# Kernel tuning notes

Hardware: AMD Instinct MI355X
Metric: run time of the kernel (lower is better)

The kernel has to match this reference:

```python
import jax, jax.numpy as jnp
import numpy as np

B, IN_DIM, OUT_DIM, N_KNOTS = 8192, 1024, 1024, 4


def setup_inputs() -> dict:
    key = jax.random.key(0)
    k_feat, k_phase, k_w = jax.random.split(key, 3)
    feats = jax.random.normal(k_feat, (B, IN_DIM), dtype=jnp.float32)
    phase = jax.random.uniform(k_phase, (B, 1), dtype=jnp.float32)  # phase in [0,1)
    x = jnp.concatenate([feats, phase], axis=1)  # [B, IN_DIM+1]
    bound = np.sqrt(6.0 / (OUT_DIM * IN_DIM))
    weight_knots = jax.random.uniform(
        k_w, (N_KNOTS, OUT_DIM, IN_DIM), dtype=jnp.float32, minval=-bound, maxval=bound)
    bias_knots = jnp.zeros((N_KNOTS, OUT_DIM), dtype=jnp.float32)
    return {"x": x, "weight_knots": weight_knots, "bias_knots": bias_knots}


def _cubic(y, mu):
    # Catmull-Rom cubic blend over the 4 gathered knots, y: [B,4,D], mu: [B,1]
    y0, y1, y2, y3 = y[:, 0], y[:, 1], y[:, 2], y[:, 3]
    return ((-0.5 * y0 + 1.5 * y1 - 1.5 * y2 + 0.5 * y3) * mu * mu * mu
            + (y0 - 2.5 * y1 + 2.0 * y2 - 0.5 * y3) * mu * mu
            + (-0.5 * y0 + 0.5 * y2) * mu + y1)


def reference(x, weight_knots, bias_knots):
    K = weight_knots.shape[0]
    phase = x[:, -1]            # [B]
    feats = x[:, :-1]           # [B, IN_DIM]
    pscale = K * phase
    mu = jnp.mod(pscale, 1.0)[:, None]                       # [B, 1]
    i1 = jnp.mod(pscale.astype(jnp.int32), K)
    idx = jnp.stack([jnp.mod(i1 - 1, K), i1,
                     jnp.mod(i1 + 1, K), jnp.mod(i1 + 2, K)], axis=1)  # [B, 4]
    # Exploit linearity: matvec against each knot matrix once, then blend.
    # Mathematically identical to cubic(W0,..,W3) @ feats + cubic(b0,..,b3).
    yk = jnp.einsum('koi,bi->bko', weight_knots, feats)      # [B, K, OUT]
    y4 = jnp.take_along_axis(yk, idx[:, :, None], axis=1)    # [B, 4, OUT]
    b4 = bias_knots[idx]                                     # [B, 4, OUT]
    res = _cubic(y4 + b4, mu)                                # cubic is linear in y
    return jax.nn.elu(res)
```

## Files before the change

kernel.cpp:

```cpp
#include <hip/hip_runtime.h>
#include <math.h>

#define IN_DIM 1024
#define OUT_DIM 1024
#define NROWS 8192
#define KDIM 4096

typedef __attribute__((ext_vector_type(8))) short bf16x8;
typedef __attribute__((ext_vector_type(4))) float f32x4;

static __device__ __forceinline__ unsigned short f2bf(float f) {
  union { float f; unsigned u; } v; v.f = f;
  unsigned u = v.u;
  return (unsigned short)((u + 0x7fffu + ((u >> 16) & 1u)) >> 16);
}

__global__ __launch_bounds__(256) void prep_a_kernel(
    const float* __restrict__ x, unsigned short* __restrict__ A4,
    float* __restrict__ coef)
{
  const int b = blockIdx.x;
  const float* xr = x + (size_t)b * (IN_DIM + 1);
  const float phase = xr[IN_DIM];
  const float ps = 4.0f * phase;
  const int ip = (int)ps;
  const int i1 = ip & 3;
  const float mu = ps - (float)ip;
  const float mu2 = mu * mu, mu3 = mu2 * mu;
  const float c0 = -0.5f * mu3 +        mu2 - 0.5f * mu;
  const float c1 =  1.5f * mu3 - 2.5f * mu2 + 1.0f;
  const float c2 = -1.5f * mu3 + 2.0f * mu2 + 0.5f * mu;
  const float c3 =  0.5f * mu3 - 0.5f * mu2;
  const int d0 = (0 - i1) & 3, d1 = (1 - i1) & 3, d2 = (2 - i1) & 3, d3 = (3 - i1) & 3;
  const float w0 = d0 == 0 ? c1 : d0 == 1 ? c2 : d0 == 2 ? c3 : c0;
  const float w1 = d1 == 0 ? c1 : d1 == 1 ? c2 : d1 == 2 ? c3 : c0;
  const float w2 = d2 == 0 ? c1 : d2 == 1 ? c2 : d2 == 2 ? c3 : c0;
  const float w3 = d3 == 0 ? c1 : d3 == 1 ? c2 : d3 == 2 ? c3 : c0;
  if (threadIdx.x == 0) {
    float4 cv; cv.x = w0; cv.y = w1; cv.z = w2; cv.w = w3;
    *reinterpret_cast<float4*>(coef + (size_t)b * 4) = cv;
  }

  const int i = threadIdx.x * 4;
  const float f0 = xr[i], f1 = xr[i + 1], f2 = xr[i + 2], f3 = xr[i + 3];
  unsigned short* arow = A4 + (size_t)b * KDIM;
  ushort4 vv;
  vv.x = f2bf(w0 * f0); vv.y = f2bf(w0 * f1); vv.z = f2bf(w0 * f2); vv.w = f2bf(w0 * f3);
  *reinterpret_cast<ushort4*>(arow + 0 * IN_DIM + i) = vv;
  vv.x = f2bf(w1 * f0); vv.y = f2bf(w1 * f1); vv.z = f2bf(w1 * f2); vv.w = f2bf(w1 * f3);
  *reinterpret_cast<ushort4*>(arow + 1 * IN_DIM + i) = vv;
  vv.x = f2bf(w2 * f0); vv.y = f2bf(w2 * f1); vv.z = f2bf(w2 * f2); vv.w = f2bf(w2 * f3);
  *reinterpret_cast<ushort4*>(arow + 2 * IN_DIM + i) = vv;
  vv.x = f2bf(w3 * f0); vv.y = f2bf(w3 * f1); vv.z = f2bf(w3 * f2); vv.w = f2bf(w3 * f3);
  *reinterpret_cast<ushort4*>(arow + 3 * IN_DIM + i) = vv;
}

__global__ __launch_bounds__(256) void prep_w_kernel(
    const float* __restrict__ W, unsigned short* __restrict__ Wb)
{
  const int t = blockIdx.x * 256 + threadIdx.x;
  const int flat = t * 4;
  const int k = flat >> 20;
  const int o = (flat >> 10) & 1023;
  const int i = flat & 1023;
  const float4 f = *reinterpret_cast<const float4*>(W + flat);
  ushort4 vv;
  vv.x = f2bf(f.x); vv.y = f2bf(f.y); vv.z = f2bf(f.z); vv.w = f2bf(f.w);
  *reinterpret_cast<ushort4*>(Wb + (size_t)o * KDIM + k * IN_DIM + i) = vv;
}

#define BM 128
#define BN 128
#define BK 64

__global__ __launch_bounds__(256, 2) void gemm_kernel(
    const unsigned short* __restrict__ A4,
    const unsigned short* __restrict__ Wb,
    const float* __restrict__ coef,
    const float* __restrict__ bias,
    float* __restrict__ out)
{
  __shared__ unsigned short As[BM * BK];
  __shared__ unsigned short Bs[BN * BK];

  const int tid  = threadIdx.x;
  const int wave = tid >> 6;
  const int lane = tid & 63;
  const int row0 = blockIdx.y * BM;
  const int col0 = blockIdx.x * BN;

  const int srow = tid >> 3;
  const int scc  = tid & 7;
  const int sgc  = (scc ^ (srow & 7)) * 8;

  const int wr  = (wave >> 1) * 64;
  const int wc  = (wave & 1) * 64;
  const int fm  = lane & 15;
  const int fq  = lane >> 4;

  f32x4 acc[4][4];
  const f32x4 zero = {0.f, 0.f, 0.f, 0.f};
  #pragma unroll
  for (int a = 0; a < 4; a++)
    #pragma unroll
    for (int b = 0; b < 4; b++)
      acc[a][b] = zero;

  const unsigned short* Abase = A4 + (size_t)row0 * KDIM;
  const unsigned short* Bbase = Wb + (size_t)col0 * KDIM;

  for (int kb = 0; kb < KDIM; kb += BK) {
    #pragma unroll
    for (int it = 0; it < 4; it++) {
      const int r = srow + it * 32;
      __builtin_amdgcn_global_load_lds(
          (const __attribute__((address_space(1))) void*)(Abase + (size_t)r * KDIM + kb + sgc),
          (__attribute__((address_space(3))) void*)(As + r * BK + scc * 8), 16, 0, 0);
      __builtin_amdgcn_global_load_lds(
          (const __attribute__((address_space(1))) void*)(Bbase + (size_t)r * KDIM + kb + sgc),
          (__attribute__((address_space(3))) void*)(Bs + r * BK + scc * 8), 16, 0, 0);
    }
    __syncthreads();

    #pragma unroll
    for (int kk = 0; kk < BK; kk += 32) {
      bf16x8 af[4], bfr[4];
      #pragma unroll
      for (int mi = 0; mi < 4; mi++) {
        const int r = wr + mi * 16 + fm;
        const int lc = ((kk >> 3) + fq) ^ (fm & 7);
        af[mi] = *reinterpret_cast<const bf16x8*>(As + r * BK + lc * 8);
      }
      #pragma unroll
      for (int ni = 0; ni < 4; ni++) {
        const int r = wc + ni * 16 + fm;
        const int lc = ((kk >> 3) + fq) ^ (fm & 7);
        bfr[ni] = *reinterpret_cast<const bf16x8*>(Bs + r * BK + lc * 8);
      }
      #pragma unroll
      for (int mi = 0; mi < 4; mi++)
        #pragma unroll
        for (int ni = 0; ni < 4; ni++)
          acc[mi][ni] = __builtin_amdgcn_mfma_f32_16x16x32_bf16(
              af[mi], bfr[ni], acc[mi][ni], 0, 0, 0);
    }
    __syncthreads();
  }

  #pragma unroll
  for (int mi = 0; mi < 4; mi++) {
    const int rbase = row0 + wr + mi * 16 + (fq << 2);
    const float4 cf0 = *reinterpret_cast<const float4*>(coef + (size_t)(rbase + 0) * 4);
    const float4 cf1 = *reinterpret_cast<const float4*>(coef + (size_t)(rbase + 1) * 4);
    const float4 cf2 = *reinterpret_cast<const float4*>(coef + (size_t)(rbase + 2) * 4);
    const float4 cf3 = *reinterpret_cast<const float4*>(coef + (size_t)(rbase + 3) * 4);
    const float4 cfs[4] = {cf0, cf1, cf2, cf3};
    #pragma unroll
    for (int ni = 0; ni < 4; ni++) {
      const int col = col0 + wc + ni * 16 + fm;
      const float b0 = bias[col];
      const float b1 = bias[OUT_DIM + col];
      const float b2 = bias[2 * OUT_DIM + col];
      const float b3 = bias[3 * OUT_DIM + col];
      #pragma unroll
      for (int r = 0; r < 4; r++) {
        float v = acc[mi][ni][r]
                + cfs[r].x * b0 + cfs[r].y * b1 + cfs[r].z * b2 + cfs[r].w * b3;
        v = (v > 0.0f) ? v : expm1f(v);
        out[(size_t)(rbase + r) * OUT_DIM + col] = v;
      }
    }
  }
}

extern "C" void kernel_launch(void* const* d_in, const int* in_sizes, int n_in,
                              void* d_out, int out_size, void* d_ws, size_t ws_size,
                              hipStream_t stream) {
  const float* x  = (const float*)d_in[0];
  const float* wk = (const float*)d_in[1];
  const float* bk = (const float*)d_in[2];
  float* out = (float*)d_out;

  char* ws = (char*)d_ws;
  float* coef          = (float*)ws;
  unsigned short* Wb   = (unsigned short*)(ws + (128u << 10));
  unsigned short* A4   = (unsigned short*)(ws + (128u << 10) + (8u << 20));

  hipLaunchKernelGGL(prep_a_kernel, dim3(NROWS), dim3(256), 0, stream, x, A4, coef);
  hipLaunchKernelGGL(prep_w_kernel, dim3(4096), dim3(256), 0, stream, wk, Wb);
  hipLaunchKernelGGL(gemm_kernel, dim3(OUT_DIM / BN, NROWS / BM), dim3(256), 0, stream,
                     A4, Wb, coef, bk, out);
}
```

Measured before the change: 190.8 us.

## Build scaled A tiles in GEMM from a bf16 feature copy instead of materializing A4

New measurement: 182.2 us. 1.05x faster.

```diff
diff --git a/kernel.cpp b/kernel.cpp
--- a/kernel.cpp
+++ b/kernel.cpp
@@ -4,7 +4,7 @@
 #define IN_DIM 1024
 #define OUT_DIM 1024
 #define NROWS 8192
-#define KDIM 4096
+#define XSTRIDE 1025
 
 typedef __attribute__((ext_vector_type(8))) short bf16x8;
 typedef __attribute__((ext_vector_type(4))) float f32x4;
@@ -15,58 +15,30 @@
   return (unsigned short)((u + 0x7fffu + ((u >> 16) & 1u)) >> 16);
 }
 
-__global__ __launch_bounds__(256) void prep_a_kernel(
-    const float* __restrict__ x, unsigned short* __restrict__ A4,
-    float* __restrict__ coef)
+__global__ __launch_bounds__(256) void prep_kernel(
+    const float* __restrict__ x, const float* __restrict__ W,
+    unsigned short* __restrict__ Wb, unsigned short* __restrict__ F)
 {
-  const int b = blockIdx.x;
-  const float* xr = x + (size_t)b * (IN_DIM + 1);
-  const float phase = xr[IN_DIM];
-  const float ps = 4.0f * phase;
-  const int ip = (int)ps;
-  const int i1 = ip & 3;
-  const float mu = ps - (float)ip;
-  const float mu2 = mu * mu, mu3 = mu2 * mu;
-  const float c0 = -0.5f * mu3 +        mu2 - 0.5f * mu;
-  const float c1 =  1.5f * mu3 - 2.5f * mu2 + 1.0f;
-  const float c2 = -1.5f * mu3 + 2.0f * mu2 + 0.5f * mu;
-  const float c3 =  0.5f * mu3 - 0.5f * mu2;
-  const int d0 = (0 - i1) & 3, d1 = (1 - i1) & 3, d2 = (2 - i1) & 3, d3 = (3 - i1) & 3;
-  const float w0 = d0 == 0 ? c1 : d0 == 1 ? c2 : d0 == 2 ? c3 : c0;
-  const float w1 = d1 == 0 ? c1 : d1 == 1 ? c2 : d1 == 2 ? c3 : c0;
-  const float w2 = d2 == 0 ? c1 : d2 == 1 ? c2 : d2 == 2 ? c3 : c0;
-  const float w3 = d3 == 0 ? c1 : d3 == 1 ? c2 : d3 == 2 ? c3 : c0;
-  if (threadIdx.x == 0) {
-    float4 cv; cv.x = w0; cv.y = w1; cv.z = w2; cv.w = w3;
-    *reinterpret_cast<float4*>(coef + (size_t)b * 4) = cv;
-  }
-
-  const int i = threadIdx.x * 4;
-  const float f0 = xr[i], f1 = xr[i + 1], f2 = xr[i + 2], f3 = xr[i + 3];
-  unsigned short* arow = A4 + (size_t)b * KDIM;
-  ushort4 vv;
-  vv.x = f2bf(w0 * f0); vv.y = f2bf(w0 * f1); vv.z = f2bf(w0 * f2); vv.w = f2bf(w0 * f3);
-  *reinterpret_cast<ushort4*>(arow + 0 * IN_DIM + i) = vv;
-  vv.x = f2bf(w1 * f0); vv.y = f2bf(w1 * f1); vv.z = f2bf(w1 * f2); vv.w = f2bf(w1 * f3);
-  *reinterpret_cast<ushort4*>(arow + 1 * IN_DIM + i) = vv;
-  vv.x = f2bf(w2 * f0); vv.y = f2bf(w2 * f1); vv.z = f2bf(w2 * f2); vv.w = f2bf(w2 * f3);
-  *reinterpret_cast<ushort4*>(arow + 2 * IN_DIM + i) = vv;
-  vv.x = f2bf(w3 * f0); vv.y = f2bf(w3 * f1); vv.z = f2bf(w3 * f2); vv.w = f2bf(w3 * f3);
-  *reinterpret_cast<ushort4*>(arow + 3 * IN_DIM + i) = vv;
-}
-
-__global__ __launch_bounds__(256) void prep_w_kernel(
-    const float* __restrict__ W, unsigned short* __restrict__ Wb)
-{
-  const int t = blockIdx.x * 256 + threadIdx.x;
-  const int flat = t * 4;
-  const int k = flat >> 20;
-  const int o = (flat >> 10) & 1023;
-  const int i = flat & 1023;
-  const float4 f = *reinterpret_cast<const float4*>(W + flat);
-  ushort4 vv;
-  vv.x = f2bf(f.x); vv.y = f2bf(f.y); vv.z = f2bf(f.z); vv.w = f2bf(f.w);
-  *reinterpret_cast<ushort4*>(Wb + (size_t)o * KDIM + k * IN_DIM + i) = vv;
+  const int blk = blockIdx.x;
+  if (blk < 4096) {
+    const int t = blk * 256 + threadIdx.x;
+    const int flat = t * 4;
+    const int k = flat >> 20;
+    const int o = (flat >> 10) & 1023;
+    const int i = flat & 1023;
+    const float4 f = *reinterpret_cast<const float4*>(W + flat);
+    ushort4 vv;
+    vv.x = f2bf(f.x); vv.y = f2bf(f.y); vv.z = f2bf(f.z); vv.w = f2bf(f.w);
+    *reinterpret_cast<ushort4*>(Wb + (size_t)o * 4096 + k * 1024 + i) = vv;
+  } else {
+    const int b = blk - 4096;
+    const float* xr = x + (size_t)b * XSTRIDE;
+    const int i = threadIdx.x * 4;
+    ushort4 vv;
+    vv.x = f2bf(xr[i]); vv.y = f2bf(xr[i + 1]);
+    vv.z = f2bf(xr[i + 2]); vv.w = f2bf(xr[i + 3]);
+    *reinterpret_cast<ushort4*>(F + (size_t)b * 1024 + i) = vv;
+  }
 }
 
 #define BM 128
@@ -74,14 +46,15 @@
 #define BK 64
 
 __global__ __launch_bounds__(256, 2) void gemm_kernel(
-    const unsigned short* __restrict__ A4,
+    const unsigned short* __restrict__ F,
     const unsigned short* __restrict__ Wb,
-    const float* __restrict__ coef,
+    const float* __restrict__ x,
     const float* __restrict__ bias,
     float* __restrict__ out)
 {
   __shared__ unsigned short As[BM * BK];
   __shared__ unsigned short Bs[BN * BK];
+  __shared__ float cfs[BM][4];
 
   const int tid  = threadIdx.x;
   const int wave = tid >> 6;
@@ -89,14 +62,39 @@
   const int row0 = blockIdx.y * BM;
   const int col0 = blockIdx.x * BN;
 
+  if (tid < BM) {
+    const float phase = x[(size_t)(row0 + tid) * XSTRIDE + IN_DIM];
+    const float ps = 4.0f * phase;
+    const int ip = (int)ps;
+    const int i1 = ip & 3;
+    const float mu = ps - (float)ip;
+    const float mu2 = mu * mu, mu3 = mu2 * mu;
+    const float c0 = -0.5f * mu3 +        mu2 - 0.5f * mu;
+    const float c1 =  1.5f * mu3 - 2.5f * mu2 + 1.0f;
+    const float c2 = -1.5f * mu3 + 2.0f * mu2 + 0.5f * mu;
+    const float c3 =  0.5f * mu3 - 0.5f * mu2;
+    const int d0 = (0 - i1) & 3, d1 = (1 - i1) & 3, d2 = (2 - i1) & 3, d3 = (3 - i1) & 3;
+    float4 cv;
+    cv.x = d0 == 0 ? c1 : d0 == 1 ? c2 : d0 == 2 ? c3 : c0;
+    cv.y = d1 == 0 ? c1 : d1 == 1 ? c2 : d1 == 2 ? c3 : c0;
+    cv.z = d2 == 0 ? c1 : d2 == 1 ? c2 : d2 == 2 ? c3 : c0;
+    cv.w = d3 == 0 ? c1 : d3 == 1 ? c2 : d3 == 2 ? c3 : c0;
+    *reinterpret_cast<float4*>(cfs[tid]) = cv;
+  }
+  __syncthreads();
+
+  const int ar  = tid >> 1;
+  const int ac0 = (tid & 1) * 32;
+  const float4 cfr = *reinterpret_cast<const float4*>(cfs[ar]);
+
   const int srow = tid >> 3;
   const int scc  = tid & 7;
   const int sgc  = (scc ^ (srow & 7)) * 8;
 
-  const int wr  = (wave >> 1) * 64;
-  const int wc  = (wave & 1) * 64;
-  const int fm  = lane & 15;
-  const int fq  = lane >> 4;
+  const int wr = (wave >> 1) * 64;
+  const int wc = (wave & 1) * 64;
+  const int fm = lane & 15;
+  const int fq = lane >> 4;
 
   f32x4 acc[4][4];
   const f32x4 zero = {0.f, 0.f, 0.f, 0.f};
@@ -106,55 +104,79 @@
     for (int b = 0; b < 4; b++)
       acc[a][b] = zero;
 
-  const unsigned short* Abase = A4 + (size_t)row0 * KDIM;
-  const unsigned short* Bbase = Wb + (size_t)col0 * KDIM;
-
-  for (int kb = 0; kb < KDIM; kb += BK) {
-    #pragma unroll
-    for (int it = 0; it < 4; it++) {
-      const int r = srow + it * 32;
-      __builtin_amdgcn_global_load_lds(
-          (const __attribute__((address_space(1))) void*)(Abase + (size_t)r * KDIM + kb + sgc),
-          (__attribute__((address_space(3))) void*)(As + r * BK + scc * 8), 16, 0, 0);
-      __builtin_amdgcn_global_load_lds(
-          (const __attribute__((address_space(1))) void*)(Bbase + (size_t)r * KDIM + kb + sgc),
-          (__attribute__((address_space(3))) void*)(Bs + r * BK + scc * 8), 16, 0, 0);
+  const unsigned short* Arow  = F + (size_t)(row0 + ar) * 1024 + ac0;
+  const unsigned short* Bbase = Wb + (size_t)col0 * 4096;
+
+  for (int kb0 = 0; kb0 < 1024; kb0 += BK) {
+    uint4 araw[4];
+    #pragma unroll
+    for (int m = 0; m < 4; m++)
+      araw[m] = *reinterpret_cast<const uint4*>(Arow + kb0 + m * 8);
+
+    #pragma unroll
+    for (int k = 0; k < 4; k++) {
+      const float ck = (k == 0) ? cfr.x : (k == 1) ? cfr.y : (k == 2) ? cfr.z : cfr.w;
+      #pragma unroll
+      for (int m = 0; m < 4; m++) {
+        uint4 d = araw[m];
+        uint4 r;
+        #pragma unroll
+        for (int j = 0; j < 4; j++) {
+          const unsigned dj = (&d.x)[j];
+          float lo = __uint_as_float(dj << 16);
+          float hi = __uint_as_float(dj & 0xffff0000u);
+          lo *= ck; hi *= ck;
+          const unsigned lr = __float_as_uint(lo) + 0x8000u;
+          const unsigned hr = __float_as_uint(hi) + 0x8000u;
+          (&r.x)[j] = __builtin_amdgcn_perm(hr, lr, 0x07060302u);
+        }
+        const int gc = (ac0 >> 3) + m;
+        const int slot = gc ^ (ar & 7);
+        *reinterpret_cast<uint4*>(As + ar * BK + slot * 8) = r;
+      }
+      #pragma unroll
+      for (int it = 0; it < 4; it++) {
+        const int rr = srow + it * 32;
+        __builtin_amdgcn_global_load_lds(
+            (const __attribute__((address_space(1))) void*)(Bbase + (size_t)rr * 4096 + k * 1024 + kb0 + sgc),
+            (__attribute__((address_space(3))) void*)(Bs + rr * BK + scc * 8), 16, 0, 0);
+      }
+      __syncthreads();
+
+      #pragma unroll
+      for (int kk = 0; kk < BK; kk += 32) {
+        bf16x8 af[4], bfr[4];
+        #pragma unroll
+        for (int mi = 0; mi < 4; mi++) {
+          const int r = wr + mi * 16 + fm;
+          const int lc = ((kk >> 3) + fq) ^ (fm & 7);
+          af[mi] = *reinterpret_cast<const bf16x8*>(As + r * BK + lc * 8);
+        }
+        #pragma unroll
+        for (int ni = 0; ni < 4; ni++) {
+          const int r = wc + ni * 16 + fm;
+          const int lc = ((kk >> 3) + fq) ^ (fm & 7);
+          bfr[ni] = *reinterpret_cast<const bf16x8*>(Bs + r * BK + lc * 8);
+        }
+        #pragma unroll
+        for (int mi = 0; mi < 4; mi++)
+          #pragma unroll
+          for (int ni = 0; ni < 4; ni++)
+            acc[mi][ni] = __builtin_amdgcn_mfma_f32_16x16x32_bf16(
+                af[mi], bfr[ni], acc[mi][ni], 0, 0, 0);
+      }
+      __syncthreads();
     }
-    __syncthreads();
-
-    #pragma unroll
-    for (int kk = 0; kk < BK; kk += 32) {
-      bf16x8 af[4], bfr[4];
-      #pragma unroll
-      for (int mi = 0; mi < 4; mi++) {
-        const int r = wr + mi * 16 + fm;
-        const int lc = ((kk >> 3) + fq) ^ (fm & 7);
-        af[mi] = *reinterpret_cast<const bf16x8*>(As + r * BK + lc * 8);
-      }
-      #pragma unroll
-      for (int ni = 0; ni < 4; ni++) {
-        const int r = wc + ni * 16 + fm;
-        const int lc = ((kk >> 3) + fq) ^ (fm & 7);
-        bfr[ni] = *reinterpret_cast<const bf16x8*>(Bs + r * BK + lc * 8);
-      }
-      #pragma unroll
-      for (int mi = 0; mi < 4; mi++)
-        #pragma unroll
-        for (int ni = 0; ni < 4; ni++)
-          acc[mi][ni] = __builtin_amdgcn_mfma_f32_16x16x32_bf16(
-              af[mi], bfr[ni], acc[mi][ni], 0, 0, 0);
-    }
-    __syncthreads();
   }
 
   #pragma unroll
   for (int mi = 0; mi < 4; mi++) {
-    const int rbase = row0 + wr + mi * 16 + (fq << 2);
-    const float4 cf0 = *reinterpret_cast<const float4*>(coef + (size_t)(rbase + 0) * 4);
-    const float4 cf1 = *reinterpret_cast<const float4*>(coef + (size_t)(rbase + 1) * 4);
-    const float4 cf2 = *reinterpret_cast<const float4*>(coef + (size_t)(rbase + 2) * 4);
-    const float4 cf3 = *reinterpret_cast<const float4*>(coef + (size_t)(rbase + 3) * 4);
-    const float4 cfs[4] = {cf0, cf1, cf2, cf3};
+    const int rloc = wr + mi * 16 + (fq << 2);
+    const int rbase = row0 + rloc;
+    float4 cfs4[4];
+    #pragma unroll
+    for (int r = 0; r < 4; r++)
+      cfs4[r] = *reinterpret_cast<const float4*>(cfs[rloc + r]);
     #pragma unroll
     for (int ni = 0; ni < 4; ni++) {
       const int col = col0 + wc + ni * 16 + fm;
@@ -165,7 +187,7 @@
       #pragma unroll
       for (int r = 0; r < 4; r++) {
         float v = acc[mi][ni][r]
-                + cfs[r].x * b0 + cfs[r].y * b1 + cfs[r].z * b2 + cfs[r].w * b3;
+                + cfs4[r].x * b0 + cfs4[r].y * b1 + cfs4[r].z * b2 + cfs4[r].w * b3;
         v = (v > 0.0f) ? v : expm1f(v);
         out[(size_t)(rbase + r) * OUT_DIM + col] = v;
       }
@@ -182,12 +204,10 @@
   float* out = (float*)d_out;
 
   char* ws = (char*)d_ws;
-  float* coef          = (float*)ws;
-  unsigned short* Wb   = (unsigned short*)(ws + (128u << 10));
-  unsigned short* A4   = (unsigned short*)(ws + (128u << 10) + (8u << 20));
-
-  hipLaunchKernelGGL(prep_a_kernel, dim3(NROWS), dim3(256), 0, stream, x, A4, coef);
-  hipLaunchKernelGGL(prep_w_kernel, dim3(4096), dim3(256), 0, stream, wk, Wb);
+  unsigned short* Wb = (unsigned short*)ws;
+  unsigned short* F  = (unsigned short*)(ws + (16u << 20));
+
+  hipLaunchKernelGGL(prep_kernel, dim3(4096 + NROWS), dim3(256), 0, stream, x, wk, Wb, F);
   hipLaunchKernelGGL(gemm_kernel, dim3(OUT_DIM / BN, NROWS / BM), dim3(256), 0, stream,
-                     A4, Wb, coef, bk, out);
-}
+                     F, Wb, x, bk, out);
+}
```

## Blend knot outputs in epilogue instead of scaling inputs along K

Applied to the files above, without the earlier changes.

Result: faster. 161.3 us (-15.4%).

```diff
diff --git a/kernel.cpp b/kernel.cpp
--- a/kernel.cpp
+++ b/kernel.cpp
@@ -4,77 +4,73 @@
 #define IN_DIM 1024
 #define OUT_DIM 1024
 #define NROWS 8192
-#define KDIM 4096
+#define XSTRIDE 1025
 
 typedef __attribute__((ext_vector_type(8))) short bf16x8;
 typedef __attribute__((ext_vector_type(4))) float f32x4;
 
-static __device__ __forceinline__ unsigned short f2bf(float f) {
+static __device__ __forceinline__ unsigned f2bf(float f) {
   union { float f; unsigned u; } v; v.f = f;
   unsigned u = v.u;
-  return (unsigned short)((u + 0x7fffu + ((u >> 16) & 1u)) >> 16);
+  return (u + 0x7fffu + ((u >> 16) & 1u)) >> 16;
 }
 
-__global__ __launch_bounds__(256) void prep_a_kernel(
-    const float* __restrict__ x, unsigned short* __restrict__ A4,
+__global__ __launch_bounds__(256) void prep_kernel(
+    const float* __restrict__ x, const float* __restrict__ W,
+    unsigned short* __restrict__ Wb, unsigned short* __restrict__ F,
     float* __restrict__ coef)
 {
-  const int b = blockIdx.x;
-  const float* xr = x + (size_t)b * (IN_DIM + 1);
-  const float phase = xr[IN_DIM];
-  const float ps = 4.0f * phase;
-  const int ip = (int)ps;
-  const int i1 = ip & 3;
-  const float mu = ps - (float)ip;
-  const float mu2 = mu * mu, mu3 = mu2 * mu;
-  const float c0 = -0.5f * mu3 +        mu2 - 0.5f * mu;
-  const float c1 =  1.5f * mu3 - 2.5f * mu2 + 1.0f;
-  const float c2 = -1.5f * mu3 + 2.0f * mu2 + 0.5f * mu;
-  const float c3 =  0.5f * mu3 - 0.5f * mu2;
-  const int d0 = (0 - i1) & 3, d1 = (1 - i1) & 3, d2 = (2 - i1) & 3, d3 = (3 - i1) & 3;
-  const float w0 = d0 == 0 ? c1 : d0 == 1 ? c2 : d0 == 2 ? c3 : c0;
-  const float w1 = d1 == 0 ? c1 : d1 == 1 ? c2 : d1 == 2 ? c3 : c0;
-  const float w2 = d2 == 0 ? c1 : d2 == 1 ? c2 : d2 == 2 ? c3 : c0;
-  const float w3 = d3 == 0 ? c1 : d3 == 1 ? c2 : d3 == 2 ? c3 : c0;
-  if (threadIdx.x == 0) {
-    float4 cv; cv.x = w0; cv.y = w1; cv.z = w2; cv.w = w3;
-    *reinterpret_cast<float4*>(coef + (size_t)b * 4) = cv;
+  const int blk = blockIdx.x;
+  if (blk < 2048) {
+    const int t = blk * 256 + threadIdx.x;
+    const int flat = t * 8;
+    const int k = flat >> 20;
+    const int o = (flat >> 10) & 1023;
+    const int i = flat & 1023;
+    const float4 fa = *reinterpret_cast<const float4*>(W + flat);
+    const float4 fb = *reinterpret_cast<const float4*>(W + flat + 4);
+    uint4 pk;
+    pk.x = f2bf(fa.x) | (f2bf(fa.y) << 16);
+    pk.y = f2bf(fa.z) | (f2bf(fa.w) << 16);
+    pk.z = f2bf(fb.x) | (f2bf(fb.y) << 16);
+    pk.w = f2bf(fb.z) | (f2bf(fb.w) << 16);
+    const int g = (o & 15) | (k << 4) | ((o >> 4) << 6);
+    *reinterpret_cast<uint4*>(Wb + (size_t)g * 1024 + i) = pk;
+  } else {
+    const int b = blk - 2048;
+    const float* xr = x + (size_t)b * XSTRIDE;
+    const int i = threadIdx.x * 4;
+    ushort4 vv;
+    vv.x = (unsigned short)f2bf(xr[i]);     vv.y = (unsigned short)f2bf(xr[i + 1]);
+    vv.z = (unsigned short)f2bf(xr[i + 2]); vv.w = (unsigned short)f2bf(xr[i + 3]);
+    *reinterpret_cast<ushort4*>(F + (size_t)b * 1024 + i) = vv;
+    if (threadIdx.x == 0) {
+      const float ps = 4.0f * xr[IN_DIM];
+      const int ip = (int)ps;
+      const int i1 = ip & 3;
+      const float mu = ps - (float)ip;
+      const float mu2 = mu * mu, mu3 = mu2 * mu;
+      const float c0 = -0.5f * mu3 +        mu2 - 0.5f * mu;
+      const float c1 =  1.5f * mu3 - 2.5f * mu2 + 1.0f;
+      const float c2 = -1.5f * mu3 + 2.0f * mu2 + 0.5f * mu;
+      const float c3 =  0.5f * mu3 - 0.5f * mu2;
+      const int d0 = (0-i1)&3, d1 = (1-i1)&3, d2 = (2-i1)&3, d3 = (3-i1)&3;
+      float4 cv;
+      cv.x = d0==0 ? c1 : d0==1 ? c2 : d0==2 ? c3 : c0;
+      cv.y = d1==0 ? c1 : d1==1 ? c2 : d1==2 ? c3 : c0;
+      cv.z = d2==0 ? c1 : d2==1 ? c2 : d2==2 ? c3 : c0;
+      cv.w = d3==0 ? c1 : d3==1 ? c2 : d3==2 ? c3 : c0;
+      *reinterpret_cast<float4*>(coef + (size_t)b * 4) = cv;
+    }
   }
-
-  const int i = threadIdx.x * 4;
-  const float f0 = xr[i], f1 = xr[i + 1], f2 = xr[i + 2], f3 = xr[i + 3];
-  unsigned short* arow = A4 + (size_t)b * KDIM;
-  ushort4 vv;
-  vv.x = f2bf(w0 * f0); vv.y = f2bf(w0 * f1); vv.z = f2bf(w0 * f2); vv.w = f2bf(w0 * f3);
-  *reinterpret_cast<ushort4*>(arow + 0 * IN_DIM + i) = vv;
-  vv.x = f2bf(w1 * f0); vv.y = f2bf(w1 * f1); vv.z = f2bf(w1 * f2); vv.w = f2bf(w1 * f3);
-  *reinterpret_cast<ushort4*>(arow + 1 * IN_DIM + i) = vv;
-  vv.x = f2bf(w2 * f0); vv.y = f2bf(w2 * f1); vv.z = f2bf(w2 * f2); vv.w = f2bf(w2 * f3);
-  *reinterpret_cast<ushort4*>(arow + 2 * IN_DIM + i) = vv;
-  vv.x = f2bf(w3 * f0); vv.y = f2bf(w3 * f1); vv.z = f2bf(w3 * f2); vv.w = f2bf(w3 * f3);
-  *reinterpret_cast<ushort4*>(arow + 3 * IN_DIM + i) = vv;
-}
-
-__global__ __launch_bounds__(256) void prep_w_kernel(
-    const float* __restrict__ W, unsigned short* __restrict__ Wb)
-{
-  const int t = blockIdx.x * 256 + threadIdx.x;
-  const int flat = t * 4;
-  const int k = flat >> 20;
-  const int o = (flat >> 10) & 1023;
-  const int i = flat & 1023;
-  const float4 f = *reinterpret_cast<const float4*>(W + flat);
-  ushort4 vv;
-  vv.x = f2bf(f.x); vv.y = f2bf(f.y); vv.z = f2bf(f.z); vv.w = f2bf(f.w);
-  *reinterpret_cast<ushort4*>(Wb + (size_t)o * KDIM + k * IN_DIM + i) = vv;
 }
 
 #define BM 128
 #define BN 128
 #define BK 64
 
-__global__ __launch_bounds__(256, 2) void gemm_kernel(
-    const unsigned short* __restrict__ A4,
+__global__ __launch_bounds__(256, 4) void gemm_kernel(
+    const unsigned short* __restrict__ F,
     const unsigned short* __restrict__ Wb,
     const float* __restrict__ coef,
     const float* __restrict__ bias,
@@ -82,21 +78,26 @@
 {
   __shared__ unsigned short As[BM * BK];
   __shared__ unsigned short Bs[BN * BK];
+  __shared__ float cfs[BM][4];
 
   const int tid  = threadIdx.x;
   const int wave = tid >> 6;
   const int lane = tid & 63;
-  const int row0 = blockIdx.y * BM;
-  const int col0 = blockIdx.x * BN;
+  const int row0  = blockIdx.y * BM;
+  const int col0g = blockIdx.x * BN;
+
+  if (tid < BM)
+    *reinterpret_cast<float4*>(cfs[tid]) =
+        *reinterpret_cast<const float4*>(coef + (size_t)(row0 + tid) * 4);
 
   const int srow = tid >> 3;
   const int scc  = tid & 7;
   const int sgc  = (scc ^ (srow & 7)) * 8;
 
-  const int wr  = (wave >> 1) * 64;
-  const int wc  = (wave & 1) * 64;
-  const int fm  = lane & 15;
-  const int fq  = lane >> 4;
+  const int wr = (wave >> 1) * 64;
+  const int wc = (wave & 1) * 64;
+  const int fm = lane & 15;
+  const int fq = lane >> 4;
 
   f32x4 acc[4][4];
   const f32x4 zero = {0.f, 0.f, 0.f, 0.f};
@@ -106,18 +107,18 @@
     for (int b = 0; b < 4; b++)
       acc[a][b] = zero;
 
-  const unsigned short* Abase = A4 + (size_t)row0 * KDIM;
-  const unsigned short* Bbase = Wb + (size_t)col0 * KDIM;
+  const unsigned short* Abase = F  + (size_t)row0  * 1024;
+  const unsigned short* Bbase = Wb + (size_t)col0g * 1024;
 
-  for (int kb = 0; kb < KDIM; kb += BK) {
+  for (int kb = 0; kb < 1024; kb += BK) {
     #pragma unroll
     for (int it = 0; it < 4; it++) {
       const int r = srow + it * 32;
       __builtin_amdgcn_global_load_lds(
-          (const __attribute__((address_space(1))) void*)(Abase + (size_t)r * KDIM + kb + sgc),
+          (const __attribute__((address_space(1))) void*)(Abase + (size_t)r * 1024 + kb + sgc),
           (__attribute__((address_space(3))) void*)(As + r * BK + scc * 8), 16, 0, 0);
       __builtin_amdgcn_global_load_lds(
-          (const __attribute__((address_space(1))) void*)(Bbase + (size_t)r * KDIM + kb + sgc),
+          (const __attribute__((address_space(1))) void*)(Bbase + (size_t)r * 1024 + kb + sgc),
           (__attribute__((address_space(3))) void*)(Bs + r * BK + scc * 8), 16, 0, 0);
     }
     __syncthreads();
@@ -127,13 +128,13 @@
       bf16x8 af[4], bfr[4];
       #pragma unroll
       for (int mi = 0; mi < 4; mi++) {
-        const int r = wr + mi * 16 + fm;
+        const int r  = wr + mi * 16 + fm;
         const int lc = ((kk >> 3) + fq) ^ (fm & 7);
         af[mi] = *reinterpret_cast<const bf16x8*>(As + r * BK + lc * 8);
       }
       #pragma unroll
       for (int ni = 0; ni < 4; ni++) {
-        const int r = wc + ni * 16 + fm;
+        const int r  = wc + ni * 16 + fm;
         const int lc = ((kk >> 3) + fq) ^ (fm & 7);
         bfr[ni] = *reinterpret_cast<const bf16x8*>(Bs + r * BK + lc * 8);
       }
@@ -147,28 +148,23 @@
     __syncthreads();
   }
 
+  const int o = fm + 16 * (2 * blockIdx.x + (wave & 1));
+  const float b0 = bias[o];
+  const float b1 = bias[OUT_DIM + o];
+  const float b2 = bias[2 * OUT_DIM + o];
+  const float b3 = bias[3 * OUT_DIM + o];
   #pragma unroll
   for (int mi = 0; mi < 4; mi++) {
-    const int rbase = row0 + wr + mi * 16 + (fq << 2);
-    const float4 cf0 = *reinterpret_cast<const float4*>(coef + (size_t)(rbase + 0) * 4);
-    const float4 cf1 = *reinterpret_cast<const float4*>(coef + (size_t)(rbase + 1) * 4);
-    const float4 cf2 = *reinterpret_cast<const float4*>(coef + (size_t)(rbase + 2) * 4);
-    const float4 cf3 = *reinterpret_cast<const float4*>(coef + (size_t)(rbase + 3) * 4);
-    const float4 cfs[4] = {cf0, cf1, cf2, cf3};
     #pragma unroll
-    for (int ni = 0; ni < 4; ni++) {
-      const int col = col0 + wc + ni * 16 + fm;
-      const float b0 = bias[col];
-      const float b1 = bias[OUT_DIM + col];
-      const float b2 = bias[2 * OUT_DIM + col];
-      const float b3 = bias[3 * OUT_DIM + col];
-      #pragma unroll
-      for (int r = 0; r < 4; r++) {
-        float v = acc[mi][ni][r]
-                + cfs[r].x * b0 + cfs[r].y * b1 + cfs[r].z * b2 + cfs[r].w * b3;
-        v = (v > 0.0f) ? v : expm1f(v);
-        out[(size_t)(rbase + r) * OUT_DIM + col] = v;
-      }
+    for (int r = 0; r < 4; r++) {
+      const int rloc = wr + mi * 16 + (fq << 2) + r;
+      const float4 c = *reinterpret_cast<const float4*>(cfs[rloc]);
+      float v = c.x * (acc[mi][0][r] + b0)
+              + c.y * (acc[mi][1][r] + b1)
+              + c.z * (acc[mi][2][r] + b2)
+              + c.w * (acc[mi][3][r] + b3);
+      v = (v > 0.0f) ? v : expm1f(v);
+      out[(size_t)(row0 + rloc) * OUT_DIM + o] = v;
     }
   }
 }
@@ -182,12 +178,12 @@
   float* out = (float*)d_out;
 
   char* ws = (char*)d_ws;
-  float* coef          = (float*)ws;
-  unsigned short* Wb   = (unsigned short*)(ws + (128u << 10));
-  unsigned short* A4   = (unsigned short*)(ws + (128u << 10) + (8u << 20));
+  unsigned short* Wb = (unsigned short*)ws;
+  unsigned short* F  = (unsigned short*)(ws + (8u << 20));
+  float* coef        = (float*)(ws + (24u << 20));
 
-  hipLaunchKernelGGL(prep_a_kernel, dim3(NROWS), dim3(256), 0, stream, x, A4, coef);
-  hipLaunchKernelGGL(prep_w_kernel, dim3(4096), dim3(256), 0, stream, wk, Wb);
-  hipLaunchKernelGGL(gemm_kernel, dim3(OUT_DIM / BN, NROWS / BM), dim3(256), 0, stream,
-                     A4, Wb, coef, bk, out);
+  hipLaunchKernelGGL(prep_kernel, dim3(2048 + NROWS), dim3(256), 0, stream,
+                     x, wk, Wb, F, coef);
+  hipLaunchKernelGGL(gemm_kernel, dim3(4096 / BN, NROWS / BM), dim3(256), 0, stream,
+                     F, Wb, coef, bk, out);
 }
```
